# Kernel optimization log

Hardware: AMD Instinct MI355X
Metric: run time of the kernel (lower is better)

## Reference

```python
import jax, jax.numpy as jnp
from jax import lax
import numpy as np

SCORE_THRESH = 0.05
NMS_THRESH = 0.5
MAX_DET = 100
MIN_SIZE = 0.01
BBOX_CLIP = float(np.log(1000.0 / 16.0))
NEG = -1e10


def setup_inputs() -> dict:
    key = jax.random.key(0)
    ks = jax.random.split(key, 12)
    N, IN, REP, C = 2000, 256 * 7 * 7, 1024, 91
    box_features = jax.random.normal(ks[0], (N, IN), jnp.float32)
    x1 = jax.random.uniform(ks[1], (N,), jnp.float32, 0.0, 1000.0)
    y1 = jax.random.uniform(ks[2], (N,), jnp.float32, 0.0, 600.0)
    bw = jax.random.uniform(ks[3], (N,), jnp.float32, 16.0, 200.0)
    bh = jax.random.uniform(ks[4], (N,), jnp.float32, 16.0, 180.0)
    proposals = jnp.stack([x1, y1, x1 + bw, y1 + bh], axis=1)
    W1 = jax.random.normal(ks[5], (IN, REP), jnp.float32) * 0.01
    b1 = jnp.zeros((REP,), jnp.float32)
    W2 = jax.random.normal(ks[6], (REP, REP), jnp.float32) * 0.03
    b2 = jnp.zeros((REP,), jnp.float32)
    Wc = jax.random.normal(ks[7], (REP, C), jnp.float32) * 0.1
    bc = jax.random.normal(ks[8], (C,), jnp.float32) * 0.5
    Wr = jax.random.normal(ks[9], (REP, 4 * C), jnp.float32) * 0.01
    br = jnp.zeros((4 * C,), jnp.float32)
    return dict(box_features=box_features, proposals=proposals,
                W1=W1, b1=b1, W2=W2, b2=b2, Wc=Wc, bc=bc, Wr=Wr, br=br,
                image_h=800, image_w=1216)


def _nms(boxes, scores):
    """Greedy NMS with fixed trip count; scores already masked to NEG for invalid."""
    M = boxes.shape[0]
    areas = (boxes[:, 2] - boxes[:, 0]) * (boxes[:, 3] - boxes[:, 1])
    idxs = jnp.arange(M)

    def step(sm, _):
        i = jnp.argmax(sm)
        valid = sm[i] > NEG * 0.5
        b = boxes[i]
        xx1 = jnp.maximum(b[0], boxes[:, 0]); yy1 = jnp.maximum(b[1], boxes[:, 1])
        xx2 = jnp.minimum(b[2], boxes[:, 2]); yy2 = jnp.minimum(b[3], boxes[:, 3])
        inter = jnp.clip(xx2 - xx1, 0.0) * jnp.clip(yy2 - yy1, 0.0)
        iou = inter / (areas[i] + areas - inter + 1e-9)
        suppress = (iou > NMS_THRESH) | (idxs == i)
        sm = jnp.where(valid, jnp.where(suppress, NEG, sm), sm)
        return sm, jnp.where(valid, i, -1)

    _, keep = lax.scan(step, scores, None, length=MAX_DET)
    return keep  # [MAX_DET] int, -1 for padding


def reference(box_features, proposals, W1, b1, W2, b2, Wc, bc, Wr, br, image_h, image_w):
    N = box_features.shape[0]
    C = Wc.shape[1]
    # box head MLP (Linear+ReLU x2) and predictors
    h = jax.nn.relu(box_features @ W1 + b1)
    h = jax.nn.relu(h @ W2 + b2)
    class_logits = h @ Wc + bc                      # [N, C]
    box_reg = (h @ Wr + br).reshape(N, C, 4)        # [N, C, 4]
    # box decode (weights 10,10,5,5) against proposals
    pw = proposals[:, 2] - proposals[:, 0]
    ph = proposals[:, 3] - proposals[:, 1]
    pcx = proposals[:, 0] + 0.5 * pw
    pcy = proposals[:, 1] + 0.5 * ph
    dx = box_reg[..., 0] / 10.0
    dy = box_reg[..., 1] / 10.0
    dw = jnp.minimum(box_reg[..., 2] / 5.0, BBOX_CLIP)
    dh = jnp.minimum(box_reg[..., 3] / 5.0, BBOX_CLIP)
    cx = dx * pw[:, None] + pcx[:, None]
    cy = dy * ph[:, None] + pcy[:, None]
    w = jnp.exp(dw) * pw[:, None]
    hh = jnp.exp(dh) * ph[:, None]
    boxes = jnp.stack([cx - 0.5 * w, cy - 0.5 * hh, cx + 0.5 * w, cy + 0.5 * hh], axis=-1)
    scores = jax.nn.softmax(class_logits, axis=-1)
    # clip to image
    Wim = jnp.float32(image_w); Him = jnp.float32(image_h)
    boxes = jnp.stack([jnp.clip(boxes[..., 0], 0.0, Wim),
                       jnp.clip(boxes[..., 1], 0.0, Him),
                       jnp.clip(boxes[..., 2], 0.0, Wim),
                       jnp.clip(boxes[..., 3], 0.0, Him)], axis=-1)
    # drop background class, flatten to [N*(C-1)]
    boxes = boxes[:, 1:].reshape(-1, 4)
    scores = scores[:, 1:].reshape(-1)
    labels = jnp.broadcast_to(jnp.arange(1, C, dtype=jnp.int32), (N, C - 1)).reshape(-1)
    # score threshold + remove small boxes (as masking, static shapes)
    bw = boxes[:, 2] - boxes[:, 0]
    bh = boxes[:, 3] - boxes[:, 1]
    valid = (scores > SCORE_THRESH) & (bw >= MIN_SIZE) & (bh >= MIN_SIZE)
    sm = jnp.where(valid, scores, NEG)
    # class-aware (batched) NMS via per-class coordinate offsets
    off = labels.astype(boxes.dtype) * (jnp.maximum(Wim, Him) + 1.0)
    keep = _nms(boxes + off[:, None], sm)
    mask = keep >= 0
    idx = jnp.maximum(keep, 0)
    out_boxes = jnp.take(boxes, idx, axis=0) * mask[:, None]
    out_scores = jnp.take(scores, idx) * mask
    out_labels = jnp.take(labels, idx) * mask.astype(jnp.int32)
    return out_boxes, out_scores, out_labels
```

## Files before the change

kernel.cpp:

```cpp
#include <hip/hip_runtime.h>

#define CPC 2000
#define SPC 100
#define NCLS 90
#define TM 128
#define TN 128
#define TKK 16

typedef __attribute__((ext_vector_type(8))) short bf16x8;
typedef __attribute__((ext_vector_type(4))) float f32x4;

__device__ __forceinline__ unsigned short f2bf_rne(float f) {
    unsigned u = __float_as_uint(f);
    return (unsigned short)((u + 0x7FFFu + ((u >> 16) & 1u)) >> 16);
}
__device__ __forceinline__ unsigned short f2bf_trunc(float f) {
    return (unsigned short)(__float_as_uint(f) >> 16);
}
__device__ __forceinline__ float bfhi_f32(float f) {
    return __uint_as_float(__float_as_uint(f) & 0xFFFF0000u);
}
__device__ __forceinline__ void async_load16(const void* g, void* l) {
    __builtin_amdgcn_global_load_lds((const __attribute__((address_space(1))) unsigned int*)g,
                                     (__attribute__((address_space(3))) unsigned int*)l, 16, 0, 0);
}
__device__ __forceinline__ int swz(int c) { return c ^ ((c >> 3) & 3); }

__global__ __launch_bounds__(256) void split_transpose(
    const float* __restrict__ W, unsigned short* __restrict__ Thi,
    unsigned short* __restrict__ Tlo, int K, int N)
{
    __shared__ float tile[32][33];
    const int kt = blockIdx.x * 32, nt = blockIdx.y * 32;
    const int tx = threadIdx.x & 31, ty = threadIdx.x >> 5;
#pragma unroll
    for (int j = 0; j < 4; ++j) {
        int k = kt + ty + j * 8, n = nt + tx;
        tile[ty + j * 8][tx] = (k < K && n < N) ? W[(size_t)k * N + n] : 0.f;
    }
    __syncthreads();
#pragma unroll
    for (int j = 0; j < 4; ++j) {
        int n = nt + ty + j * 8, k = kt + tx;
        if (n < N && k < K) {
            float f = tile[tx][ty + j * 8];
            Thi[(size_t)n * K + k] = f2bf_trunc(f);
            Tlo[(size_t)n * K + k] = f2bf_rne(f - bfhi_f32(f));
        }
    }
}

__global__ __launch_bounds__(256) void split_transpose2(
    const float* __restrict__ Wa, const float* __restrict__ Wb, int Na, int Nb,
    unsigned short* __restrict__ Thi, unsigned short* __restrict__ Tlo, int K)
{
    const int N = Na + Nb;
    __shared__ float tile[32][33];
    const int kt = blockIdx.x * 32, nt = blockIdx.y * 32;
    const int tx = threadIdx.x & 31, ty = threadIdx.x >> 5;
#pragma unroll
    for (int j = 0; j < 4; ++j) {
        int k = kt + ty + j * 8, n = nt + tx;
        float v = 0.f;
        if (k < K && n < N)
            v = (n < Na) ? Wa[(size_t)k * Na + n] : Wb[(size_t)k * Nb + (n - Na)];
        tile[ty + j * 8][tx] = v;
    }
    __syncthreads();
#pragma unroll
    for (int j = 0; j < 4; ++j) {
        int n = nt + ty + j * 8, k = kt + tx;
        if (n < N && k < K) {
            float f = tile[tx][ty + j * 8];
            Thi[(size_t)n * K + k] = f2bf_trunc(f);
            Tlo[(size_t)n * K + k] = f2bf_rne(f - bfhi_f32(f));
        }
    }
}

__global__ __launch_bounds__(256, 4) void gemm_bf16x3_f32a(
    const float* __restrict__ A, const unsigned short* __restrict__ Bhi,
    const unsigned short* __restrict__ Blo, float* __restrict__ C,
    int M, int N, int K, int klen)
{
    __shared__ unsigned short Ah[2048], Al[2048], Bh[4096], Bl[4096];
    const int tid = threadIdx.x;
    const int wv = tid >> 6, ln = tid & 63;
    const int q = ln >> 4, lm = ln & 15;
    const int m0 = blockIdx.y * 64, n0 = blockIdx.x * 128;
    const int k0 = blockIdx.z * klen, k1 = k0 + klen;
    const int bcol_t = wv * 32;

    f32x4 acc[4][2];
#pragma unroll
    for (int i = 0; i < 4; ++i)
#pragma unroll
        for (int j = 0; j < 2; ++j) acc[i][j] = (f32x4)0.f;

    const int r = tid >> 2, h = tid & 3;
    int gr = m0 + r; if (gr >= M) gr = M - 1;
    const float* Arow = A + (size_t)gr * K + h * 8;
    const int apc = swz(tid);

    unsigned bsrc[2];
#pragma unroll
    for (int i = 0; i < 2; ++i) {
        int s = i * 256 + tid;
        int gn = n0 + (s >> 2); if (gn >= N) gn = N - 1;
        int qe = (s & 3) ^ ((s >> 3) & 3);
        bsrc[i] = (unsigned)gn * (unsigned)K + (unsigned)(qe * 8);
    }

    for (int kt = k0; kt < k1; kt += 32) {
#pragma unroll
        for (int i = 0; i < 2; ++i) {
            async_load16(Bhi + bsrc[i] + kt, &Bh[(i * 256 + wv * 64) * 8]);
            async_load16(Blo + bsrc[i] + kt, &Bl[(i * 256 + wv * 64) * 8]);
        }
        float4 v0 = *reinterpret_cast<const float4*>(Arow + kt);
        float4 v1 = *reinterpret_cast<const float4*>(Arow + kt + 4);
        float f[8] = {v0.x, v0.y, v0.z, v0.w, v1.x, v1.y, v1.z, v1.w};
        bf16x8 hi, lo;
#pragma unroll
        for (int e = 0; e < 8; ++e) {
            hi[e] = (short)f2bf_trunc(f[e]);
            lo[e] = (short)f2bf_rne(f[e] - bfhi_f32(f[e]));
        }
        *(bf16x8*)&Ah[apc * 8] = hi;
        *(bf16x8*)&Al[apc * 8] = lo;
        __syncthreads();

        bf16x8 afh[4], afl[4], bfh[2], bfl[2];
#pragma unroll
        for (int mi = 0; mi < 4; ++mi) {
            int p = swz((mi * 16 + lm) * 4 + q);
            afh[mi] = *(const bf16x8*)&Ah[p * 8];
            afl[mi] = *(const bf16x8*)&Al[p * 8];
        }
#pragma unroll
        for (int ni = 0; ni < 2; ++ni) {
            int p = swz((bcol_t + ni * 16 + lm) * 4 + q);
            bfh[ni] = *(const bf16x8*)&Bh[p * 8];
            bfl[ni] = *(const bf16x8*)&Bl[p * 8];
        }
#pragma unroll
        for (int mi = 0; mi < 4; ++mi)
#pragma unroll
            for (int ni = 0; ni < 2; ++ni) {
                acc[mi][ni] = __builtin_amdgcn_mfma_f32_16x16x32_bf16(afh[mi], bfh[ni], acc[mi][ni], 0, 0, 0);
                acc[mi][ni] = __builtin_amdgcn_mfma_f32_16x16x32_bf16(afl[mi], bfh[ni], acc[mi][ni], 0, 0, 0);
                acc[mi][ni] = __builtin_amdgcn_mfma_f32_16x16x32_bf16(afh[mi], bfl[ni], acc[mi][ni], 0, 0, 0);
            }
        __syncthreads();
    }

    float* Cz = C + (size_t)blockIdx.z * (size_t)M * (size_t)N;
#pragma unroll
    for (int mi = 0; mi < 4; ++mi)
#pragma unroll
        for (int ni = 0; ni < 2; ++ni)
#pragma unroll
            for (int ri = 0; ri < 4; ++ri) {
                int rr = m0 + mi * 16 + q * 4 + ri;
                int cc = n0 + bcol_t + ni * 16 + lm;
                if (rr < M && cc < N) Cz[(size_t)rr * N + cc] = acc[mi][ni][ri];
            }
}

__global__ __launch_bounds__(256, 4) void gemm_bf16x3_sa(
    const unsigned short* __restrict__ Ahi_g, const unsigned short* __restrict__ Alo_g,
    const unsigned short* __restrict__ Bhi, const unsigned short* __restrict__ Blo,
    float* __restrict__ C, int M, int N, int K, int klen)
{
    __shared__ unsigned short Ah[2048], Al[2048], Bh[4096], Bl[4096];
    const int tid = threadIdx.x;
    const int wv = tid >> 6, ln = tid & 63;
    const int q = ln >> 4, lm = ln & 15;
    const int m0 = blockIdx.y * 64, n0 = blockIdx.x * 128;
    const int k0 = blockIdx.z * klen, k1 = k0 + klen;
    const int bcol_t = wv * 32;

    f32x4 acc[4][2];
#pragma unroll
    for (int i = 0; i < 4; ++i)
#pragma unroll
        for (int j = 0; j < 2; ++j) acc[i][j] = (f32x4)0.f;

    {
    }
    int agr = m0 + (tid >> 2); if (agr >= M) agr = M - 1;
    const int aqe = (tid & 3) ^ ((tid >> 3) & 3);
    const unsigned asrc = (unsigned)agr * (unsigned)K + (unsigned)(aqe * 8);

    unsigned bsrc[2];
#pragma unroll
    for (int i = 0; i < 2; ++i) {
        int s = i * 256 + tid;
        int gn = n0 + (s >> 2); if (gn >= N) gn = N - 1;
        int qe = (s & 3) ^ ((s >> 3) & 3);
        bsrc[i] = (unsigned)gn * (unsigned)K + (unsigned)(qe * 8);
    }

    for (int kt = k0; kt < k1; kt += 32) {
        async_load16(Ahi_g + asrc + kt, &Ah[(wv * 64) * 8]);
        async_load16(Alo_g + asrc + kt, &Al[(wv * 64) * 8]);
#pragma unroll
        for (int i = 0; i < 2; ++i) {
            async_load16(Bhi + bsrc[i] + kt, &Bh[(i * 256 + wv * 64) * 8]);
            async_load16(Blo + bsrc[i] + kt, &Bl[(i * 256 + wv * 64) * 8]);
        }
        __syncthreads();

        bf16x8 afh[4], afl[4], bfh[2], bfl[2];
#pragma unroll
        for (int mi = 0; mi < 4; ++mi) {
            int p = swz((mi * 16 + lm) * 4 + q);
            afh[mi] = *(const bf16x8*)&Ah[p * 8];
            afl[mi] = *(const bf16x8*)&Al[p * 8];
        }
#pragma unroll
        for (int ni = 0; ni < 2; ++ni) {
            int p = swz((bcol_t + ni * 16 + lm) * 4 + q);
            bfh[ni] = *(const bf16x8*)&Bh[p * 8];
            bfl[ni] = *(const bf16x8*)&Bl[p * 8];
        }
#pragma unroll
        for (int mi = 0; mi < 4; ++mi)
#pragma unroll
            for (int ni = 0; ni < 2; ++ni) {
                acc[mi][ni] = __builtin_amdgcn_mfma_f32_16x16x32_bf16(afh[mi], bfh[ni], acc[mi][ni], 0, 0, 0);
                acc[mi][ni] = __builtin_amdgcn_mfma_f32_16x16x32_bf16(afl[mi], bfh[ni], acc[mi][ni], 0, 0, 0);
                acc[mi][ni] = __builtin_amdgcn_mfma_f32_16x16x32_bf16(afh[mi], bfl[ni], acc[mi][ni], 0, 0, 0);
            }
        __syncthreads();
    }

    float* Cz = C + (size_t)blockIdx.z * (size_t)M * (size_t)N;
#pragma unroll
    for (int mi = 0; mi < 4; ++mi)
#pragma unroll
        for (int ni = 0; ni < 2; ++ni)
#pragma unroll
            for (int ri = 0; ri < 4; ++ri) {
                int rr = m0 + mi * 16 + q * 4 + ri;
                int cc = n0 + bcol_t + ni * 16 + lm;
                if (rr < M && cc < N) Cz[(size_t)rr * N + cc] = acc[mi][ni][ri];
            }
}

__global__ __launch_bounds__(256) void gemm_f32(
    const float* __restrict__ A, const float* __restrict__ B,
    const float* __restrict__ bias, float* __restrict__ C,
    int M, int N, int K, int ksplit, int relu)
{
    __shared__ float As[TKK][TM + 4];
    __shared__ float Bs[TKK][TN + 4];
    const int tid = threadIdx.x;
    const int tx = tid & 15, ty = tid >> 4;
    const int m0 = blockIdx.y * TM, n0 = blockIdx.x * TN;
    const int z = blockIdx.z;
    const int kstart = z * ksplit;
    const int kend = (kstart + ksplit < K) ? (kstart + ksplit) : K;
    float* Cz = C + (size_t)z * (size_t)M * (size_t)N;
    const bool nvec = ((N & 3) == 0);

    float acc[8][8];
#pragma unroll
    for (int i = 0; i < 8; ++i)
#pragma unroll
        for (int j = 0; j < 8; ++j) acc[i][j] = 0.f;

    for (int kt = kstart; kt < kend; kt += TKK) {
#pragma unroll
        for (int l = 0; l < 2; ++l) {
            int idx = tid + l * 256;
            int rr = idx >> 2, kq = idx & 3;
            float4 v = make_float4(0.f, 0.f, 0.f, 0.f);
            int grr = m0 + rr;
            if (grr < M)
                v = *reinterpret_cast<const float4*>(A + (size_t)grr * K + kt + (kq << 2));
            As[(kq << 2) + 0][rr] = v.x;
            As[(kq << 2) + 1][rr] = v.y;
            As[(kq << 2) + 2][rr] = v.z;
            As[(kq << 2) + 3][rr] = v.w;
        }
#pragma unroll
        for (int l = 0; l < 2; ++l) {
            int idx = tid + l * 256;
            int kk = idx >> 5, nq = idx & 31;
            int gn = n0 + (nq << 2);
            const float* bp = B + (size_t)(kt + kk) * N + gn;
            float4 v;
            if (nvec && gn + 3 < N) {
                v = *reinterpret_cast<const float4*>(bp);
            } else {
                v.x = (gn + 0 < N) ? bp[0] : 0.f;
                v.y = (gn + 1 < N) ? bp[1] : 0.f;
                v.z = (gn + 2 < N) ? bp[2] : 0.f;
                v.w = (gn + 3 < N) ? bp[3] : 0.f;
            }
            *reinterpret_cast<float4*>(&Bs[kk][nq << 2]) = v;
        }
        __syncthreads();
#pragma unroll
        for (int kk = 0; kk < TKK; ++kk) {
            float a[8], b[8];
            *reinterpret_cast<float4*>(&a[0]) = *reinterpret_cast<const float4*>(&As[kk][ty * 8]);
            *reinterpret_cast<float4*>(&a[4]) = *reinterpret_cast<const float4*>(&As[kk][ty * 8 + 4]);
            *reinterpret_cast<float4*>(&b[0]) = *reinterpret_cast<const float4*>(&Bs[kk][tx * 4]);
            *reinterpret_cast<float4*>(&b[4]) = *reinterpret_cast<const float4*>(&Bs[kk][64 + tx * 4]);
#pragma unroll
            for (int i = 0; i < 8; ++i)
#pragma unroll
                for (int j = 0; j < 8; ++j)
                    acc[i][j] = fmaf(a[i], b[j], acc[i][j]);
        }
        __syncthreads();
    }
#pragma unroll
    for (int i = 0; i < 8; ++i) {
        int grr = m0 + ty * 8 + i;
        if (grr >= M) continue;
#pragma unroll
        for (int j = 0; j < 8; ++j) {
            int gc = n0 + ((j < 4) ? (tx * 4 + j) : (64 + tx * 4 + (j - 4)));
            if (gc >= N) continue;
            float v = acc[i][j];
            if (bias) v += bias[gc];
            if (relu) v = fmaxf(v, 0.f);
            Cz[(size_t)grr * N + gc] = v;
        }
    }
}

__global__ void combine_bias_act(const float* __restrict__ P, const float* __restrict__ bias,
                                 float* __restrict__ H, int total, int N, int nsplit,
                                 int pstride, int relu)
{
    int i = blockIdx.x * blockDim.x + threadIdx.x;
    if (i >= total) return;
    float s = P[i];
    for (int j = 1; j < nsplit; ++j) s += P[i + (size_t)j * (size_t)pstride];
    s += bias[i % N];
    if (relu) s = fmaxf(s, 0.f);
    H[i] = s;
}

__global__ void combine_bias_split(const float* __restrict__ P, const float* __restrict__ bias,
                                   unsigned short* __restrict__ Hhi, unsigned short* __restrict__ Hlo,
                                   int total, int N, int nsplit, int pstride, int relu)
{
    int i = blockIdx.x * blockDim.x + threadIdx.x;
    if (i >= total) return;
    float s = P[i];
    for (int j = 1; j < nsplit; ++j) s += P[i + (size_t)j * (size_t)pstride];
    s += bias[i % N];
    if (relu) s = fmaxf(s, 0.f);
    Hhi[i] = f2bf_trunc(s);
    Hlo[i] = f2bf_rne(s - bfhi_f32(s));
}

__global__ void combine_head(const float* __restrict__ P, const float* __restrict__ bc,
                             const float* __restrict__ br, float* __restrict__ H,
                             int total, int nsplit, int pstride)
{
    int i = blockIdx.x * blockDim.x + threadIdx.x;
    if (i >= total) return;
    float s = P[i];
    for (int j = 1; j < nsplit; ++j) s += P[i + (size_t)j * (size_t)pstride];
    int col = i % 455;
    s += (col < 91) ? bc[col] : br[col - 91];
    H[i] = s;
}

__device__ __forceinline__ float scalar_dim(const int* p)
{
    int iv = *p;
    return (iv > 0 && iv < (1 << 20)) ? (float)iv : *reinterpret_cast<const float*>(p);
}

__global__ __launch_bounds__(128) void decode_compact(
    const float* __restrict__ logits, int lstr, const float* __restrict__ breg, int bstr,
    const float4* __restrict__ proposals, const int* __restrict__ ihp,
    const int* __restrict__ iwp,
    float4* __restrict__ cbox, float* __restrict__ cscore, int* __restrict__ cn,
    int* __restrict__ ccnt)
{
    const int n = blockIdx.x;
    const int c = threadIdx.x;
    __shared__ float sl[91];
    __shared__ float s_max, s_sum;
    if (c < 91) sl[c] = logits[(size_t)n * lstr + c];
    __syncthreads();
    if (c == 0) {
        float m = sl[0];
        for (int i = 1; i < 91; ++i) m = fmaxf(m, sl[i]);
        float s = 0.f;
        for (int i = 0; i < 91; ++i) s += expf(sl[i] - m);
        s_max = m; s_sum = s;
    }
    __syncthreads();
    if (c < 1 || c >= 91) return;

    const float score = expf(sl[c] - s_max) / s_sum;
    const float Wim = scalar_dim(iwp), Him = scalar_dim(ihp);
    float4 p = proposals[n];
    float pw = p.z - p.x, ph = p.w - p.y;
    float pcx = p.x + 0.5f * pw, pcy = p.y + 0.5f * ph;
    const float* r4 = breg + (size_t)n * bstr + c * 4;
    float dxv = r4[0] / 10.f, dyv = r4[1] / 10.f;
    const float BCLIP = 4.135166556742356f;
    float dwv = fminf(r4[2] / 5.f, BCLIP);
    float dhv = fminf(r4[3] / 5.f, BCLIP);
    float cx = dxv * pw + pcx, cy = dyv * ph + pcy;
    float w = expf(dwv) * pw, hh = expf(dhv) * ph;
    float x1 = cx - 0.5f * w, y1 = cy - 0.5f * hh;
    float x2 = cx + 0.5f * w, y2 = cy + 0.5f * hh;
    x1 = fminf(fmaxf(x1, 0.f), Wim);
    y1 = fminf(fmaxf(y1, 0.f), Him);
    x2 = fminf(fmaxf(x2, 0.f), Wim);
    y2 = fminf(fmaxf(y2, 0.f), Him);
    float bw = x2 - x1, bh = y2 - y1;
    if (score > 0.05f && bw >= 0.01f && bh >= 0.01f) {
        int cls = c - 1;
        int pos = atomicAdd(&ccnt[cls], 1);
        if (pos < CPC) {
            cbox[cls * CPC + pos] = make_float4(x1, y1, x2, y2);
            cscore[cls * CPC + pos] = score;
            cn[cls * CPC + pos] = n;
        }
    }
}

__global__ __launch_bounds__(256) void nms_class(
    const float4* __restrict__ cbox, const float* __restrict__ cscore,
    const int* __restrict__ cn, const int* __restrict__ ccnt,
    float4* __restrict__ sbox, float* __restrict__ sscore,
    unsigned long long* __restrict__ skey, int* __restrict__ scnt)
{
    const int cls = blockIdx.x;
    const int tid = threadIdx.x;
    int cnt = ccnt[cls]; if (cnt > CPC) cnt = CPC;

    __shared__ float4 cb[CPC];
    __shared__ unsigned long long keys[CPC];
    __shared__ unsigned long long red[4];
    __shared__ float4 selsh;
    __shared__ int selidx_sh;

    for (int i = tid; i < cnt; i += 256) {
        cb[i] = cbox[cls * CPC + i];
        unsigned int sb = __float_as_uint(cscore[cls * CPC + i]);
        sb ^= (sb >> 31) ? 0xFFFFFFFFu : 0x80000000u;
        unsigned int flat = (unsigned)cn[cls * CPC + i] * 90u + (unsigned)cls;
        keys[i] = ((unsigned long long)sb << 32) | (unsigned long long)(0xFFFFFFFFu - flat);
    }
    __syncthreads();

    int sel = 0;
    while (sel < SPC) {
        unsigned long long best = 0ull;
        for (int i = tid; i < cnt; i += 256) {
            unsigned long long k = keys[i];
            if (k > best) best = k;
        }
#pragma unroll
        for (int d = 32; d >= 1; d >>= 1) {
            unsigned long long o = __shfl_down(best, d, 64);
            if (o > best) best = o;
        }
        if ((tid & 63) == 0) red[tid >> 6] = best;
        __syncthreads();
        unsigned long long gbest = red[0];
        if (red[1] > gbest) gbest = red[1];
        if (red[2] > gbest) gbest = red[2];
        if (red[3] > gbest) gbest = red[3];
        if (gbest == 0ull) break;
        for (int i = tid; i < cnt; i += 256)
            if (keys[i] == gbest) { selsh = cb[i]; selidx_sh = i; }
        __syncthreads();
        float4 s = selsh;
        const int si = selidx_sh;
        const float sa = (s.z - s.x) * (s.w - s.y);
        if (tid == 0) {
            sbox[cls * SPC + sel] = s;
            unsigned int sb = (unsigned int)(gbest >> 32);
            sb ^= (sb >> 31) ? 0x80000000u : 0xFFFFFFFFu;
            sscore[cls * SPC + sel] = __uint_as_float(sb);
            skey[cls * SPC + sel] = gbest;
        }
        for (int i = tid; i < cnt; i += 256) {
            float4 b = cb[i];
            float xx1 = fmaxf(s.x, b.x), yy1 = fmaxf(s.y, b.y);
            float xx2 = fminf(s.z, b.z), yy2 = fminf(s.w, b.w);
            float inter = fmaxf(xx2 - xx1, 0.f) * fmaxf(yy2 - yy1, 0.f);
            float area = (b.z - b.x) * (b.w - b.y);
            if (3.f * inter > sa + area + 1e-9f || i == si) keys[i] = 0ull;
        }
        ++sel;
        __syncthreads();
    }
    if (tid == 0) scnt[cls] = sel;
}

__global__ __launch_bounds__(128) void nms_merge(
    const float4* __restrict__ sbox, const float* __restrict__ sscore,
    const unsigned long long* __restrict__ skey, const int* __restrict__ scnt,
    float* __restrict__ out)
{
    const int tid = threadIdx.x;
    __shared__ int head[NCLS];
    __shared__ unsigned long long red[2];
    __shared__ int selc_sh;
    if (tid < NCLS) head[tid] = 0;
    __syncthreads();

    for (int k = 0; k < 100; ++k) {
        unsigned long long key = 0ull;
        if (tid < NCLS && head[tid] < scnt[tid]) key = skey[tid * SPC + head[tid]];
        unsigned long long mykey = key;
#pragma unroll
        for (int d = 32; d >= 1; d >>= 1) {
            unsigned long long o = __shfl_down(key, d, 64);
            if (o > key) key = o;
        }
        if ((tid & 63) == 0) red[tid >> 6] = key;
        if (tid == 0) selc_sh = -1;
        __syncthreads();
        unsigned long long gbest = red[0] > red[1] ? red[0] : red[1];
        if (gbest != 0ull && mykey == gbest) selc_sh = tid;
        __syncthreads();
        const int c = selc_sh;
        if (tid == 0) {
            if (c >= 0) {
                int h = head[c];
                float4 b = sbox[c * SPC + h];
                out[k * 4 + 0] = b.x; out[k * 4 + 1] = b.y;
                out[k * 4 + 2] = b.z; out[k * 4 + 3] = b.w;
                out[400 + k] = sscore[c * SPC + h];
                out[500 + k] = (float)(c + 1);
            } else {
                out[k * 4 + 0] = 0.f; out[k * 4 + 1] = 0.f;
                out[k * 4 + 2] = 0.f; out[k * 4 + 3] = 0.f;
                out[400 + k] = 0.f; out[500 + k] = 0.f;
            }
        }
        if (c >= 0 && tid == c) head[c]++;
        __syncthreads();
    }
}

extern "C" void kernel_launch(void* const* d_in, const int* in_sizes, int n_in,
                              void* d_out, int out_size, void* d_ws, size_t ws_size,
                              hipStream_t stream)
{
    const float* bf    = (const float*)d_in[0];
    const float* props = (const float*)d_in[1];
    const float* W1    = (const float*)d_in[2];
    const float* b1    = (const float*)d_in[3];
    const float* W2    = (const float*)d_in[4];
    const float* b2    = (const float*)d_in[5];
    const float* Wc    = (const float*)d_in[6];
    const float* bc    = (const float*)d_in[7];
    const float* Wr    = (const float*)d_in[8];
    const float* br    = (const float*)d_in[9];
    const int*   ihp   = (const int*)d_in[10];
    const int*   iwp   = (const int*)d_in[11];
    float* ws  = (float*)d_ws;
    float* out = (float*)d_out;

    const size_t MN   = 2000ull * 1024ull;
    const size_t NLOG = 2000ull * 91ull;
    const size_t NREG = 2000ull * 364ull;
    const size_t NHEAD = 2000ull * 455ull;
    const size_t ws_floats = ws_size / 4;

    const size_t BT1F = 1024ull * 12544ull / 2;
    const size_t WT2F = 1024ull * 1024ull / 2;
    const size_t WHF  = 455ull * 1024ull / 2;
    const size_t NMSF = (size_t)NCLS * CPC * 6 + (size_t)NCLS * SPC * 7 + 256;
    const size_t PF   = 4 * MN;
    const size_t NEED = 2 * BT1F + 2 * WT2F + 2 * WHF + 2 * MN + NHEAD + NMSF + PF + 64;

    if (ws_floats >= NEED) {
        unsigned short* BT1hi = (unsigned short*)ws;
        unsigned short* BT1lo = (unsigned short*)(ws + BT1F);
        unsigned short* WT2hi = (unsigned short*)(ws + 2 * BT1F);
        unsigned short* WT2lo = (unsigned short*)(ws + 2 * BT1F + WT2F);
        unsigned short* WHhi  = (unsigned short*)(ws + 2 * BT1F + 2 * WT2F);
        unsigned short* WHlo  = (unsigned short*)(ws + 2 * BT1F + 2 * WT2F + WHF);
        float* H1   = ws + 2 * BT1F + 2 * WT2F + 2 * WHF;
        float* H2   = H1 + MN;
        float* HEAD = H2 + MN;
        float* CBOX   = HEAD + NHEAD;
        float* CSCORE = CBOX + (size_t)NCLS * CPC * 4;
        int*   CN     = (int*)(CSCORE + (size_t)NCLS * CPC);
        float* SBOX   = (float*)(CN + (size_t)NCLS * CPC);
        float* SSCORE = SBOX + (size_t)NCLS * SPC * 4;
        unsigned long long* SKEY = (unsigned long long*)(SSCORE + (size_t)NCLS * SPC);
        int*   CCNT = (int*)(SKEY + (size_t)NCLS * SPC);
        int*   SCNT = CCNT + NCLS;
        float* P = (float*)(SCNT + NCLS + 62);

        unsigned short* H1hi = (unsigned short*)H1;
        unsigned short* H1lo = H1hi + MN;
        unsigned short* H2hi = (unsigned short*)H2;
        unsigned short* H2lo = H2hi + MN;

        split_transpose<<<dim3(392, 32), 256, 0, stream>>>(W1, BT1hi, BT1lo, 12544, 1024);
        split_transpose<<<dim3(32, 32), 256, 0, stream>>>(W2, WT2hi, WT2lo, 1024, 1024);
        split_transpose2<<<dim3(32, 15), 256, 0, stream>>>(Wc, Wr, 91, 364, WHhi, WHlo, 1024);
        gemm_bf16x3_f32a<<<dim3(8, 32, 4), 256, 0, stream>>>(bf, BT1hi, BT1lo, P,
                                                             2000, 1024, 12544, 3136);
        combine_bias_split<<<(int)((MN + 255) / 256), 256, 0, stream>>>(P, b1, H1hi, H1lo,
                                                             (int)MN, 1024, 4, (int)MN, 1);
        gemm_bf16x3_sa<<<dim3(8, 32, 4), 256, 0, stream>>>(H1hi, H1lo, WT2hi, WT2lo, P,
                                                           2000, 1024, 1024, 256);
        combine_bias_split<<<(int)((MN + 255) / 256), 256, 0, stream>>>(P, b2, H2hi, H2lo,
                                                             (int)MN, 1024, 4, (int)MN, 1);
        gemm_bf16x3_sa<<<dim3(4, 32, 8), 256, 0, stream>>>(H2hi, H2lo, WHhi, WHlo, P,
                                                           2000, 455, 1024, 128);
        combine_head<<<(int)((NHEAD + 255) / 256), 256, 0, stream>>>(P, bc, br, HEAD,
                                                             (int)NHEAD, 8, (int)NHEAD);
        hipMemsetAsync(CCNT, 0, 2 * NCLS * sizeof(int), stream);
        decode_compact<<<2000, 128, 0, stream>>>(HEAD, 455, HEAD + 91, 455,
                                                 (const float4*)props, ihp, iwp,
                                                 (float4*)CBOX, CSCORE, CN, CCNT);
        nms_class<<<NCLS, 256, 0, stream>>>((const float4*)CBOX, CSCORE, CN, CCNT,
                                            (float4*)SBOX, SSCORE, SKEY, SCNT);
        nms_merge<<<1, 128, 0, stream>>>((const float4*)SBOX, SSCORE, SKEY, SCNT, out);
        return;
    }

    const size_t NMSF2 = (size_t)NCLS * CPC * 6 + (size_t)NCLS * SPC * 7 + 256;
    const size_t TAILF = 2 * MN + NLOG + NREG + NMSF2;
    int z1 = 2;
    if (ws_floats >= TAILF + 8 * MN) z1 = 8;
    else if (ws_floats >= TAILF + 4 * MN) z1 = 4;
    const size_t REUSE = (size_t)z1 * MN;
    int zh = (REUSE >= 8 * NREG) ? 8 : 4;

    float* P      = ws;
    float* H1     = P + REUSE;
    float* H2     = H1 + MN;
    float* LOG    = H2 + MN;
    float* BREG   = LOG + NLOG;
    float* CBOX   = BREG + NREG;
    float* CSCORE = CBOX + (size_t)NCLS * CPC * 4;
    int*   CN     = (int*)(CSCORE + (size_t)NCLS * CPC);
    float* SBOX   = (float*)(CN + (size_t)NCLS * CPC);
    float* SSCORE = SBOX + (size_t)NCLS * SPC * 4;
    unsigned long long* SKEY = (unsigned long long*)(SSCORE + (size_t)NCLS * SPC);
    int*   CCNT   = (int*)(SKEY + (size_t)NCLS * SPC);
    int*   SCNT   = CCNT + NCLS;

    gemm_f32<<<dim3(8, 16, z1), 256, 0, stream>>>(bf, W1, nullptr, P,
                                                  2000, 1024, 12544, 12544 / z1, 0);
    combine_bias_act<<<(int)((MN + 255) / 256), 256, 0, stream>>>(P, b1, H1,
                                                  (int)MN, 1024, z1, (int)MN, 1);
    gemm_f32<<<dim3(8, 16, 4), 256, 0, stream>>>(H1, W2, nullptr, P,
                                                 2000, 1024, 1024, 256, 0);
    combine_bias_act<<<(int)((MN + 255) / 256), 256, 0, stream>>>(P, b2, H2,
                                                 (int)MN, 1024, 4, (int)MN, 1);
    gemm_f32<<<dim3(1, 16, zh), 256, 0, stream>>>(H2, Wc, nullptr, P,
                                                  2000, 91, 1024, 1024 / zh, 0);
    combine_bias_act<<<(int)((NLOG + 255) / 256), 256, 0, stream>>>(P, bc, LOG,
                                                  (int)NLOG, 91, zh, (int)NLOG, 0);
    gemm_f32<<<dim3(3, 16, zh), 256, 0, stream>>>(H2, Wr, nullptr, P,
                                                  2000, 364, 1024, 1024 / zh, 0);
    combine_bias_act<<<(int)((NREG + 255) / 256), 256, 0, stream>>>(P, br, BREG,
                                                  (int)NREG, 364, zh, (int)NREG, 0);
    hipMemsetAsync(CCNT, 0, 2 * NCLS * sizeof(int), stream);
    decode_compact<<<2000, 128, 0, stream>>>(LOG, 91, BREG, 364,
                                             (const float4*)props, ihp, iwp,
                                             (float4*)CBOX, CSCORE, CN, CCNT);
    nms_class<<<NCLS, 256, 0, stream>>>((const float4*)CBOX, CSCORE, CN, CCNT,
                                        (float4*)SBOX, SSCORE, SKEY, SCNT);
    nms_merge<<<1, 128, 0, stream>>>((const float4*)SBOX, SSCORE, SKEY, SCNT, out);
}
```

Before: 751.0 us.

## Double-buffer LDS tiles in split-bf16 GEMMs and rebalance split-K factors

Both bf16x3 GEMM kernels now use ping-pong LDS buffers, issuing the global-to-LDS loads for the next K tile before running the MFMAs on the current one, with a single barrier per step. LDS per block doubles, so occupancy hints drop from 4 to 3 blocks per CU. Split-K factors are lowered (4→3, 8→6), with K bounds clamped for the uneven last slice, and the combine kernels are updated to match. The aim is to hide load latency behind compute and cut partial-sum traffic, at the risk of lower occupancy and fewer blocks in the grid.

```diff
diff --git a/kernel.cpp b/kernel.cpp
--- a/kernel.cpp
+++ b/kernel.cpp
@@ -26,6 +26,75 @@
 }
 __device__ __forceinline__ int swz(int c) { return c ^ ((c >> 3) & 3); }
 
+__device__ __forceinline__ void split8(const float* f, bf16x8& hi, bf16x8& lo) {
+#pragma unroll
+    for (int e = 0; e < 8; ++e) {
+        hi[e] = (short)f2bf_trunc(f[e]);
+        lo[e] = (short)f2bf_rne(f[e] - bfhi_f32(f[e]));
+    }
+}
+
+__device__ __forceinline__ void stage_b(
+    const unsigned short* __restrict__ Bhi, const unsigned short* __restrict__ Blo,
+    unsigned bsrc0, unsigned bsrc1, int ks, int wv,
+    unsigned short* BhB, unsigned short* BlB)
+{
+    async_load16(Bhi + bsrc0 + ks, &BhB[(wv * 64) * 8]);
+    async_load16(Blo + bsrc0 + ks, &BlB[(wv * 64) * 8]);
+    async_load16(Bhi + bsrc1 + ks, &BhB[(256 + wv * 64) * 8]);
+    async_load16(Blo + bsrc1 + ks, &BlB[(256 + wv * 64) * 8]);
+}
+
+__device__ __forceinline__ void stage_a_f32(
+    const float* __restrict__ Arow, int ks, int apc,
+    unsigned short* AhB, unsigned short* AlB)
+{
+    float4 v0 = *reinterpret_cast<const float4*>(Arow + ks);
+    float4 v1 = *reinterpret_cast<const float4*>(Arow + ks + 4);
+    float ff[8] = {v0.x, v0.y, v0.z, v0.w, v1.x, v1.y, v1.z, v1.w};
+    bf16x8 hi, lo;
+    split8(ff, hi, lo);
+    *(bf16x8*)&AhB[apc * 8] = hi;
+    *(bf16x8*)&AlB[apc * 8] = lo;
+}
+
+__device__ __forceinline__ void stage_a_pre(
+    const unsigned short* __restrict__ Ahi_g, const unsigned short* __restrict__ Alo_g,
+    unsigned asrc, int ks, int wv,
+    unsigned short* AhB, unsigned short* AlB)
+{
+    async_load16(Ahi_g + asrc + ks, &AhB[(wv * 64) * 8]);
+    async_load16(Alo_g + asrc + ks, &AlB[(wv * 64) * 8]);
+}
+
+__device__ __forceinline__ void mfma_tile(
+    const unsigned short* __restrict__ AhB, const unsigned short* __restrict__ AlB,
+    const unsigned short* __restrict__ BhB, const unsigned short* __restrict__ BlB,
+    int lm, int q, int bcol_t, f32x4 (&acc)[4][2])
+{
+    bf16x8 afh[4], afl[4], bfh[2], bfl[2];
+#pragma unroll
+    for (int mi = 0; mi < 4; ++mi) {
+        int p = swz((mi * 16 + lm) * 4 + q);
+        afh[mi] = *(const bf16x8*)&AhB[p * 8];
+        afl[mi] = *(const bf16x8*)&AlB[p * 8];
+    }
+#pragma unroll
+    for (int ni = 0; ni < 2; ++ni) {
+        int p = swz((bcol_t + ni * 16 + lm) * 4 + q);
+        bfh[ni] = *(const bf16x8*)&BhB[p * 8];
+        bfl[ni] = *(const bf16x8*)&BlB[p * 8];
+    }
+#pragma unroll
+    for (int mi = 0; mi < 4; ++mi)
+#pragma unroll
+        for (int ni = 0; ni < 2; ++ni) {
+            acc[mi][ni] = __builtin_amdgcn_mfma_f32_16x16x32_bf16(afh[mi], bfh[ni], acc[mi][ni], 0, 0, 0);
+            acc[mi][ni] = __builtin_amdgcn_mfma_f32_16x16x32_bf16(afl[mi], bfh[ni], acc[mi][ni], 0, 0, 0);
+            acc[mi][ni] = __builtin_amdgcn_mfma_f32_16x16x32_bf16(afh[mi], bfl[ni], acc[mi][ni], 0, 0, 0);
+        }
+}
+
 __global__ __launch_bounds__(256) void split_transpose(
     const float* __restrict__ W, unsigned short* __restrict__ Thi,
     unsigned short* __restrict__ Tlo, int K, int N)
@@ -78,17 +147,19 @@
     }
 }
 
-__global__ __launch_bounds__(256, 4) void gemm_bf16x3_f32a(
+__global__ __launch_bounds__(256, 3) void gemm_bf16x3_f32a(
     const float* __restrict__ A, const unsigned short* __restrict__ Bhi,
     const unsigned short* __restrict__ Blo, float* __restrict__ C,
     int M, int N, int K, int klen)
 {
-    __shared__ unsigned short Ah[2048], Al[2048], Bh[4096], Bl[4096];
+    __shared__ unsigned short Ah[2][2048], Al[2][2048];
+    __shared__ unsigned short Bh[2][4096], Bl[2][4096];
     const int tid = threadIdx.x;
     const int wv = tid >> 6, ln = tid & 63;
     const int q = ln >> 4, lm = ln & 15;
     const int m0 = blockIdx.y * 64, n0 = blockIdx.x * 128;
-    const int k0 = blockIdx.z * klen, k1 = k0 + klen;
+    const int k0 = blockIdx.z * klen;
+    int k1 = k0 + klen; if (k1 > K) k1 = K;
     const int bcol_t = wv * 32;
 
     f32x4 acc[4][2];
@@ -97,61 +168,43 @@
 #pragma unroll
         for (int j = 0; j < 2; ++j) acc[i][j] = (f32x4)0.f;
 
-    const int r = tid >> 2, h = tid & 3;
-    int gr = m0 + r; if (gr >= M) gr = M - 1;
-    const float* Arow = A + (size_t)gr * K + h * 8;
+    int gr = m0 + (tid >> 2); if (gr >= M) gr = M - 1;
+    const float* Arow = A + (size_t)gr * K + (tid & 3) * 8;
     const int apc = swz(tid);
 
-    unsigned bsrc[2];
-#pragma unroll
-    for (int i = 0; i < 2; ++i) {
-        int s = i * 256 + tid;
-        int gn = n0 + (s >> 2); if (gn >= N) gn = N - 1;
-        int qe = (s & 3) ^ ((s >> 3) & 3);
-        bsrc[i] = (unsigned)gn * (unsigned)K + (unsigned)(qe * 8);
-    }
-
-    for (int kt = k0; kt < k1; kt += 32) {
-#pragma unroll
-        for (int i = 0; i < 2; ++i) {
-            async_load16(Bhi + bsrc[i] + kt, &Bh[(i * 256 + wv * 64) * 8]);
-            async_load16(Blo + bsrc[i] + kt, &Bl[(i * 256 + wv * 64) * 8]);
-        }
-        float4 v0 = *reinterpret_cast<const float4*>(Arow + kt);
-        float4 v1 = *reinterpret_cast<const float4*>(Arow + kt + 4);
-        float f[8] = {v0.x, v0.y, v0.z, v0.w, v1.x, v1.y, v1.z, v1.w};
-        bf16x8 hi, lo;
-#pragma unroll
-        for (int e = 0; e < 8; ++e) {
-            hi[e] = (short)f2bf_trunc(f[e]);
-            lo[e] = (short)f2bf_rne(f[e] - bfhi_f32(f[e]));
-        }
-        *(bf16x8*)&Ah[apc * 8] = hi;
-        *(bf16x8*)&Al[apc * 8] = lo;
-        __syncthreads();
-
-        bf16x8 afh[4], afl[4], bfh[2], bfl[2];
-#pragma unroll
-        for (int mi = 0; mi < 4; ++mi) {
-            int p = swz((mi * 16 + lm) * 4 + q);
-            afh[mi] = *(const bf16x8*)&Ah[p * 8];
-            afl[mi] = *(const bf16x8*)&Al[p * 8];
-        }
-#pragma unroll
-        for (int ni = 0; ni < 2; ++ni) {
-            int p = swz((bcol_t + ni * 16 + lm) * 4 + q);
-            bfh[ni] = *(const bf16x8*)&Bh[p * 8];
-            bfl[ni] = *(const bf16x8*)&Bl[p * 8];
-        }
-#pragma unroll
-        for (int mi = 0; mi < 4; ++mi)
-#pragma unroll
-            for (int ni = 0; ni < 2; ++ni) {
-                acc[mi][ni] = __builtin_amdgcn_mfma_f32_16x16x32_bf16(afh[mi], bfh[ni], acc[mi][ni], 0, 0, 0);
-                acc[mi][ni] = __builtin_amdgcn_mfma_f32_16x16x32_bf16(afl[mi], bfh[ni], acc[mi][ni], 0, 0, 0);
-                acc[mi][ni] = __builtin_amdgcn_mfma_f32_16x16x32_bf16(afh[mi], bfl[ni], acc[mi][ni], 0, 0, 0);
-            }
-        __syncthreads();
+    unsigned bsrc0, bsrc1;
+    {
+        int s0 = tid;
+        int gn0 = n0 + (s0 >> 2); if (gn0 >= N) gn0 = N - 1;
+        bsrc0 = (unsigned)gn0 * (unsigned)K + (unsigned)(((s0 & 3) ^ ((s0 >> 3) & 3)) * 8);
+        int s1 = 256 + tid;
+        int gn1 = n0 + (s1 >> 2); if (gn1 >= N) gn1 = N - 1;
+        bsrc1 = (unsigned)gn1 * (unsigned)K + (unsigned)(((s1 & 3) ^ ((s1 >> 3) & 3)) * 8);
+    }
+
+    stage_b(Bhi, Blo, bsrc0, bsrc1, k0, wv, Bh[0], Bl[0]);
+    stage_a_f32(Arow, k0, apc, Ah[0], Al[0]);
+    __syncthreads();
+
+    int kt = k0;
+    for (;;) {
+        const bool n1 = kt + 32 < k1;
+        if (n1) {
+            stage_b(Bhi, Blo, bsrc0, bsrc1, kt + 32, wv, Bh[1], Bl[1]);
+            stage_a_f32(Arow, kt + 32, apc, Ah[1], Al[1]);
+        }
+        mfma_tile(Ah[0], Al[0], Bh[0], Bl[0], lm, q, bcol_t, acc);
+        __syncthreads();
+        if (!n1) break;
+        const bool n2 = kt + 64 < k1;
+        if (n2) {
+            stage_b(Bhi, Blo, bsrc0, bsrc1, kt + 64, wv, Bh[0], Bl[0]);
+            stage_a_f32(Arow, kt + 64, apc, Ah[0], Al[0]);
+        }
+        mfma_tile(Ah[1], Al[1], Bh[1], Bl[1], lm, q, bcol_t, acc);
+        __syncthreads();
+        if (!n2) break;
+        kt += 64;
     }
 
     float* Cz = C + (size_t)blockIdx.z * (size_t)M * (size_t)N;
@@ -167,17 +220,19 @@
             }
 }
 
-__global__ __launch_bounds__(256, 4) void gemm_bf16x3_sa(
+__global__ __launch_bounds__(256, 3) void gemm_bf16x3_sa(
     const unsigned short* __restrict__ Ahi_g, const unsigned short* __restrict__ Alo_g,
     const unsigned short* __restrict__ Bhi, const unsigned short* __restrict__ Blo,
     float* __restrict__ C, int M, int N, int K, int klen)
 {
-    __shared__ unsigned short Ah[2048], Al[2048], Bh[4096], Bl[4096];
+    __shared__ unsigned short Ah[2][2048], Al[2][2048];
+    __shared__ unsigned short Bh[2][4096], Bl[2][4096];
     const int tid = threadIdx.x;
     const int wv = tid >> 6, ln = tid & 63;
     const int q = ln >> 4, lm = ln & 15;
     const int m0 = blockIdx.y * 64, n0 = blockIdx.x * 128;
-    const int k0 = blockIdx.z * klen, k1 = k0 + klen;
+    const int k0 = blockIdx.z * klen;
+    int k1 = k0 + klen; if (k1 > K) k1 = K;
     const int bcol_t = wv * 32;
 
     f32x4 acc[4][2];
@@ -186,53 +241,43 @@
 #pragma unroll
         for (int j = 0; j < 2; ++j) acc[i][j] = (f32x4)0.f;
 
+    int agr = m0 + (tid >> 2); if (agr >= M) agr = M - 1;
+    const unsigned asrc = (unsigned)agr * (unsigned)K
+                        + (unsigned)(((tid & 3) ^ ((tid >> 3) & 3)) * 8);
+
+    unsigned bsrc0, bsrc1;
     {
-    }
-    int agr = m0 + (tid >> 2); if (agr >= M) agr = M - 1;
-    const int aqe = (tid & 3) ^ ((tid >> 3) & 3);
-    const unsigned asrc = (unsigned)agr * (unsigned)K + (unsigned)(aqe * 8);
-
-    unsigned bsrc[2];
-#pragma unroll
-    for (int i = 0; i < 2; ++i) {
-        int s = i * 256 + tid;
-        int gn = n0 + (s >> 2); if (gn >= N) gn = N - 1;
-        int qe = (s & 3) ^ ((s >> 3) & 3);
-        bsrc[i] = (unsigned)gn * (unsigned)K + (unsigned)(qe * 8);
-    }
-
-    for (int kt = k0; kt < k1; kt += 32) {
-        async_load16(Ahi_g + asrc + kt, &Ah[(wv * 64) * 8]);
-        async_load16(Alo_g + asrc + kt, &Al[(wv * 64) * 8]);
-#pragma unroll
-        for (int i = 0; i < 2; ++i) {
-            async_load16(Bhi + bsrc[i] + kt, &Bh[(i * 256 + wv * 64) * 8]);
-            async_load16(Blo + bsrc[i] + kt, &Bl[(i * 256 + wv * 64) * 8]);
-        }
-        __syncthreads();
-
-        bf16x8 afh[4], afl[4], bfh[2], bfl[2];
-#pragma unroll
-        for (int mi = 0; mi < 4; ++mi) {
-            int p = swz((mi * 16 + lm) * 4 + q);
-            afh[mi] = *(const bf16x8*)&Ah[p * 8];
-            afl[mi] = *(const bf16x8*)&Al[p * 8];
-        }
-#pragma unroll
-        for (int ni = 0; ni < 2; ++ni) {
-            int p = swz((bcol_t + ni * 16 + lm) * 4 + q);
-            bfh[ni] = *(const bf16x8*)&Bh[p * 8];
-            bfl[ni] = *(const bf16x8*)&Bl[p * 8];
-        }
-#pragma unroll
-        for (int mi = 0; mi < 4; ++mi)
-#pragma unroll
-            for (int ni = 0; ni < 2; ++ni) {
-                acc[mi][ni] = __builtin_amdgcn_mfma_f32_16x16x32_bf16(afh[mi], bfh[ni], acc[mi][ni], 0, 0, 0);
-                acc[mi][ni] = __builtin_amdgcn_mfma_f32_16x16x32_bf16(afl[mi], bfh[ni], acc[mi][ni], 0, 0, 0);
-                acc[mi][ni] = __builtin_amdgcn_mfma_f32_16x16x32_bf16(afh[mi], bfl[ni], acc[mi][ni], 0, 0, 0);
-            }
-        __syncthreads();
+        int s0 = tid;
+        int gn0 = n0 + (s0 >> 2); if (gn0 >= N) gn0 = N - 1;
+        bsrc0 = (unsigned)gn0 * (unsigned)K + (unsigned)(((s0 & 3) ^ ((s0 >> 3) & 3)) * 8);
+        int s1 = 256 + tid;
+        int gn1 = n0 + (s1 >> 2); if (gn1 >= N) gn1 = N - 1;
+        bsrc1 = (unsigned)gn1 * (unsigned)K + (unsigned)(((s1 & 3) ^ ((s1 >> 3) & 3)) * 8);
+    }
+
+    stage_b(Bhi, Blo, bsrc0, bsrc1, k0, wv, Bh[0], Bl[0]);
+    stage_a_pre(Ahi_g, Alo_g, asrc, k0, wv, Ah[0], Al[0]);
+    __syncthreads();
+
+    int kt = k0;
+    for (;;) {
+        const bool n1 = kt + 32 < k1;
+        if (n1) {
+            stage_b(Bhi, Blo, bsrc0, bsrc1, kt + 32, wv, Bh[1], Bl[1]);
+            stage_a_pre(Ahi_g, Alo_g, asrc, kt + 32, wv, Ah[1], Al[1]);
+        }
+        mfma_tile(Ah[0], Al[0], Bh[0], Bl[0], lm, q, bcol_t, acc);
+        __syncthreads();
+        if (!n1) break;
+        const bool n2 = kt + 64 < k1;
+        if (n2) {
+            stage_b(Bhi, Blo, bsrc0, bsrc1, kt + 64, wv, Bh[0], Bl[0]);
+            stage_a_pre(Ahi_g, Alo_g, asrc, kt + 64, wv, Ah[0], Al[0]);
+        }
+        mfma_tile(Ah[1], Al[1], Bh[1], Bl[1], lm, q, bcol_t, acc);
+        __syncthreads();
+        if (!n2) break;
+        kt += 64;
     }
 
     float* Cz = C + (size_t)blockIdx.z * (size_t)M * (size_t)N;
@@ -610,18 +655,18 @@
         split_transpose<<<dim3(392, 32), 256, 0, stream>>>(W1, BT1hi, BT1lo, 12544, 1024);
         split_transpose<<<dim3(32, 32), 256, 0, stream>>>(W2, WT2hi, WT2lo, 1024, 1024);
         split_transpose2<<<dim3(32, 15), 256, 0, stream>>>(Wc, Wr, 91, 364, WHhi, WHlo, 1024);
-        gemm_bf16x3_f32a<<<dim3(8, 32, 4), 256, 0, stream>>>(bf, BT1hi, BT1lo, P,
-                                                             2000, 1024, 12544, 3136);
+        gemm_bf16x3_f32a<<<dim3(8, 32, 3), 256, 0, stream>>>(bf, BT1hi, BT1lo, P,
+                                                             2000, 1024, 12544, 4192);
         combine_bias_split<<<(int)((MN + 255) / 256), 256, 0, stream>>>(P, b1, H1hi, H1lo,
-                                                             (int)MN, 1024, 4, (int)MN, 1);
-        gemm_bf16x3_sa<<<dim3(8, 32, 4), 256, 0, stream>>>(H1hi, H1lo, WT2hi, WT2lo, P,
-                                                           2000, 1024, 1024, 256);
+                                                             (int)MN, 1024, 3, (int)MN, 1);
+        gemm_bf16x3_sa<<<dim3(8, 32, 3), 256, 0, stream>>>(H1hi, H1lo, WT2hi, WT2lo, P,
+                                                           2000, 1024, 1024, 352);
         combine_bias_split<<<(int)((MN + 255) / 256), 256, 0, stream>>>(P, b2, H2hi, H2lo,
-                                                             (int)MN, 1024, 4, (int)MN, 1);
-        gemm_bf16x3_sa<<<dim3(4, 32, 8), 256, 0, stream>>>(H2hi, H2lo, WHhi, WHlo, P,
-                                                           2000, 455, 1024, 128);
+                                                             (int)MN, 1024, 3, (int)MN, 1);
+        gemm_bf16x3_sa<<<dim3(4, 32, 6), 256, 0, stream>>>(H2hi, H2lo, WHhi, WHlo, P,
+                                                           2000, 455, 1024, 192);
         combine_head<<<(int)((NHEAD + 255) / 256), 256, 0, stream>>>(P, bc, br, HEAD,
-                                                             (int)NHEAD, 8, (int)NHEAD);
+                                                             (int)NHEAD, 6, (int)NHEAD);
         hipMemsetAsync(CCNT, 0, 2 * NCLS * sizeof(int), stream);
         decode_compact<<<2000, 128, 0, stream>>>(HEAD, 455, HEAD + 91, 455,
                                                  (const float4*)props, ihp, iwp,
```

New measurement: 760.6 us. No clear change (+1.3%).
